# Optimization experiments

Hardware: AMD Instinct MI355X
Metric: run time of the kernel (lower is better)

Reference implementation:

```python
import jax, jax.numpy as jnp
import numpy as np

B, S, E, H = 64, 256, 1024, 16
D = E // H  # head dim = 64


def setup_inputs() -> dict:
    key = jax.random.key(0)
    ks = jax.random.split(key, 6)
    x = jax.random.normal(ks[0], (B, S, E), dtype=jnp.float32)
    # torch nn.MultiheadAttention packed in-projection [3E, E] and biases
    sc = 1.0 / np.sqrt(E)
    in_proj_w = jax.random.normal(ks[1], (3 * E, E), dtype=jnp.float32) * sc
    in_proj_b = jax.random.normal(ks[2], (3 * E,), dtype=jnp.float32) * 0.02
    out_proj_w = jax.random.normal(ks[3], (E, E), dtype=jnp.float32) * sc
    out_proj_b = jax.random.normal(ks[4], (E,), dtype=jnp.float32) * 0.02
    # spatial bias = exp(-dist^2 / (2*median)) in (0, 1], symmetric
    pos = jax.random.normal(ks[5], (S, 3), dtype=jnp.float32)
    dist = jnp.sqrt(jnp.sum((pos[:, None, :] - pos[None, :, :]) ** 2, -1) + 1e-12)
    med = jnp.median(dist)
    spatial_bias = jnp.exp(-dist ** 2 / (2.0 * med))
    return {"x": x, "in_proj_w": in_proj_w, "in_proj_b": in_proj_b,
            "out_proj_w": out_proj_w, "out_proj_b": out_proj_b,
            "spatial_bias": spatial_bias}


def reference(x, in_proj_w, in_proj_b, out_proj_w, out_proj_b, spatial_bias):
    # packed QKV projection: x [B,S,E] @ in_proj_w.T [E,3E]
    qkv = x @ in_proj_w.T + in_proj_b          # [B,S,3E]
    q, k, v = jnp.split(qkv, 3, axis=-1)       # each [B,S,E]
    q = q.reshape(B, S, H, D)
    k = k.reshape(B, S, H, D)
    v = v.reshape(B, S, H, D)
    scale = 1.0 / jnp.sqrt(jnp.asarray(D, dtype=x.dtype))
    # additive float attn_mask broadcast over batch & heads
    scores = jnp.einsum('bqhd,bkhd->bhqk', q, k) * scale + spatial_bias[None, None]
    attn = jax.nn.softmax(scores, axis=-1)     # [B,H,S,S]
    ctx = jnp.einsum('bhqk,bkhd->bqhd', attn, v).reshape(B, S, E)
    h = ctx @ out_proj_w.T + out_proj_b        # [B,S,E]
    return x + h
```

## Files before the change

kernel.cpp:

```cpp
#include <hip/hip_runtime.h>
#include <hip/hip_bf16.h>
#include <stdint.h>


typedef __attribute__((ext_vector_type(8))) __bf16 bf16x8;
typedef __attribute__((ext_vector_type(4))) float f32x4;

#define DEVI static __device__ __forceinline__

DEVI unsigned short f2bf(float f) {
  union { float f; unsigned u; } x; x.f = f;
  unsigned r = x.u + 0x7fffu + ((x.u >> 16) & 1u);
  return (unsigned short)(r >> 16);
}

typedef unsigned int __attribute__((address_space(1))) u32_g;
typedef unsigned int __attribute__((address_space(3))) u32_l;

DEVI void g2l16(const unsigned short* g, unsigned short* l) {
  __builtin_amdgcn_global_load_lds((const u32_g*)g, (u32_l*)l, 16, 0, 0);
}

__global__ __launch_bounds__(256) void cvt_kernel(const float* __restrict__ s,
                                                  unsigned short* __restrict__ d, int n) {
  int i = (blockIdx.x * 256 + threadIdx.x) * 4;
  if (i >= n) return;
  float4 v = *(const float4*)(s + i);
  ushort4 o;
  o.x = f2bf(v.x); o.y = f2bf(v.y); o.z = f2bf(v.z); o.w = f2bf(v.w);
  *(ushort4*)(d + i) = o;
}

template <int EPI>
__global__ __launch_bounds__(512, 2)
void gemm8(const unsigned short* __restrict__ A,
           const unsigned short* __restrict__ Bw,
           const float* __restrict__ bias,
           unsigned short* __restrict__ Qo,
           unsigned short* __restrict__ Ko,
           unsigned short* __restrict__ VTo,
           const float* __restrict__ Xres,
           float* __restrict__ Out) {
  extern __shared__ unsigned short lds[];
  const int lane = threadIdx.x & 63, wid = threadIdx.x >> 6;
  const int l15 = lane & 15, lg = lane >> 4;
  const int wr = wid >> 2, wcn = wid & 3;
  const int am0 = blockIdx.x * 256, bn0 = blockIdx.y * 256;

  const int srow0 = wid * 16 + (lane >> 2);
  const int scb0  = (lane & 3) * 16;

  f32x4 acc[8][4] = {};

#define SWZ(row) ((((row) >> 1) & 3) << 4)

#define STAGE(s) { \
    const int slot_ = (s) & 3; \
    _Pragma("unroll") \
    for (int j = 0; j < 2; ++j) { \
      const int row_ = j * 128 + srow0; \
      const int cs_ = scb0 ^ SWZ(row_); \
      g2l16(A  + (size_t)(am0 + row_) * 1024 + (s) * 32 + (cs_ >> 1), \
            &lds[slot_ * 8192 + j * 4096 + wid * 512]); \
      g2l16(Bw + (size_t)(bn0 + row_) * 1024 + (s) * 32 + (cs_ >> 1), \
            &lds[32768 + slot_ * 8192 + j * 4096 + wid * 512]); \
    } }

#define LOADFRAGS(p) \
    bf16x8 a[8], b[4]; \
    { const unsigned short* As_ = &lds[((p) & 3) * 8192]; \
      const unsigned short* Bs_ = &lds[32768 + ((p) & 3) * 8192]; \
      _Pragma("unroll") \
      for (int mf = 0; mf < 8; ++mf) { \
        const int row_ = wr * 128 + mf * 16 + l15; \
        a[mf] = *(const bf16x8*)((const char*)As_ + row_ * 64 + ((lg * 16) ^ SWZ(row_))); \
      } \
      _Pragma("unroll") \
      for (int nf = 0; nf < 4; ++nf) { \
        const int row_ = wcn * 64 + nf * 16 + l15; \
        b[nf] = *(const bf16x8*)((const char*)Bs_ + row_ * 64 + ((lg * 16) ^ SWZ(row_))); \
      } }

#define MFMAS() { \
    __builtin_amdgcn_s_setprio(1); \
    _Pragma("unroll") \
    for (int mf = 0; mf < 8; ++mf) \
      _Pragma("unroll") \
      for (int nf = 0; nf < 4; ++nf) \
        acc[mf][nf] = __builtin_amdgcn_mfma_f32_16x16x32_bf16(a[mf], b[nf], acc[mf][nf], 0, 0, 0); \
    __builtin_amdgcn_s_setprio(0); }

  STAGE(0) STAGE(1) STAGE(2)
  asm volatile("s_waitcnt vmcnt(8)" ::: "memory");
  __builtin_amdgcn_s_barrier();

#pragma unroll 4
  for (int p = 0; p < 29; ++p) {
    LOADFRAGS(p)
    STAGE(p + 3)
    asm volatile("s_waitcnt vmcnt(8)" ::: "memory");
    asm volatile("s_waitcnt lgkmcnt(0)" ::: "memory");
    __builtin_amdgcn_s_barrier();
    MFMAS()
  }
  { LOADFRAGS(29)
    asm volatile("s_waitcnt vmcnt(4)" ::: "memory");
    asm volatile("s_waitcnt lgkmcnt(0)" ::: "memory");
    __builtin_amdgcn_s_barrier();
    MFMAS() }
  { LOADFRAGS(30)
    asm volatile("s_waitcnt vmcnt(0)" ::: "memory");
    asm volatile("s_waitcnt lgkmcnt(0)" ::: "memory");
    __builtin_amdgcn_s_barrier();
    MFMAS() }
  { LOADFRAGS(31)
    MFMAS() }

  if (EPI == 0) {
#pragma unroll
    for (int nf = 0; nf < 4; ++nf) {
      const int col = bn0 + wcn * 64 + nf * 16 + l15;
      const int which = col >> 10;
      const int e = col & 1023;
      const int hh = e >> 6, dd = e & 63;
      const float bv = bias[col];
#pragma unroll
      for (int mf = 0; mf < 8; ++mf) {
        const int row0 = am0 + wr * 128 + mf * 16 + lg * 4;
        const int bb = row0 >> 8;
        const int s0 = row0 & 255;
        if (which == 2) {
          unsigned long long pk = 0;
#pragma unroll
          for (int r = 0; r < 4; ++r)
            pk |= (unsigned long long)f2bf(acc[mf][nf][r] + bv) << (16 * r);
          *(unsigned long long*)&VTo[((size_t)(bb * 16 + hh) * 64 + dd) * 256 + s0] = pk;
        } else {
          unsigned short* dst = (which == 0) ? Qo : Ko;
#pragma unroll
          for (int r = 0; r < 4; ++r)
            dst[((size_t)(bb * 16 + hh) * 256 + s0 + r) * 64 + dd] = f2bf(acc[mf][nf][r] + bv);
        }
      }
    }
  } else {
#pragma unroll
    for (int nf = 0; nf < 4; ++nf) {
      const int col = bn0 + wcn * 64 + nf * 16 + l15;
      const float bv = bias[col];
#pragma unroll
      for (int mf = 0; mf < 8; ++mf) {
#pragma unroll
        for (int r = 0; r < 4; ++r) {
          const int row = am0 + wr * 128 + mf * 16 + lg * 4 + r;
          const size_t idx = (size_t)row * 1024 + col;
          Out[idx] = Xres[idx] + acc[mf][nf][r] + bv;
        }
      }
    }
  }
#undef SWZ
#undef STAGE
#undef LOADFRAGS
#undef MFMAS
}

__global__ __launch_bounds__(256) void attn_kernel(const unsigned short* __restrict__ Qg,
                                                   const unsigned short* __restrict__ Kg,
                                                   const unsigned short* __restrict__ VTg,
                                                   const float* __restrict__ bias,
                                                   unsigned short* __restrict__ ctx) {
  __shared__ unsigned short P[4][64][80];
  const int lane = threadIdx.x & 63, wave = threadIdx.x >> 6;
  const int l15 = lane & 15, lg = lane >> 4;
  const int bh = blockIdx.x;
  const int bb = bh >> 4, hh = bh & 15;
  const size_t base = (size_t)bh * (256 * 64);
  const int q0 = wave * 64;

  bf16x8 qfr[4][2];
#pragma unroll
  for (int qi = 0; qi < 4; ++qi)
#pragma unroll
    for (int kc = 0; kc < 2; ++kc)
      qfr[qi][kc] = *(const bf16x8*)&Qg[base + (size_t)(q0 + qi * 16 + l15) * 64 + kc * 32 + lg * 8];

  f32x4 o[4][4] = {};
  float mrow[4], lrow[4];
#pragma unroll
  for (int i = 0; i < 4; ++i) { mrow[i] = -1e30f; lrow[i] = 0.f; }

  for (int c = 0; c < 4; ++c) {
    bf16x8 kfr[4][2];
#pragma unroll
    for (int kr = 0; kr < 4; ++kr)
#pragma unroll
      for (int kc = 0; kc < 2; ++kc)
        kfr[kr][kc] = *(const bf16x8*)&Kg[base + (size_t)(c * 64 + kr * 16 + l15) * 64 + kc * 32 + lg * 8];

    f32x4 s[4][4] = {};
#pragma unroll
    for (int kr = 0; kr < 4; ++kr)
#pragma unroll
      for (int qi = 0; qi < 4; ++qi)
#pragma unroll
        for (int kc = 0; kc < 2; ++kc)
          s[kr][qi] = __builtin_amdgcn_mfma_f32_16x16x32_bf16(kfr[kr][kc], qfr[qi][kc], s[kr][qi], 0, 0, 0);

    float cmax[4];
#pragma unroll
    for (int qi = 0; qi < 4; ++qi) cmax[qi] = -1e30f;
#pragma unroll
    for (int kr = 0; kr < 4; ++kr)
#pragma unroll
      for (int qi = 0; qi < 4; ++qi) {
        const int krow0 = c * 64 + kr * 16 + lg * 4;
        const int qcol = q0 + qi * 16 + l15;
        const f32x4 b4 = *(const f32x4*)&bias[qcol * 256 + krow0];
#pragma unroll
        for (int r = 0; r < 4; ++r) {
          float v = s[kr][qi][r] * 0.125f + b4[r];
          s[kr][qi][r] = v;
          cmax[qi] = fmaxf(cmax[qi], v);
        }
      }
#pragma unroll
    for (int qi = 0; qi < 4; ++qi) {
      cmax[qi] = fmaxf(cmax[qi], __shfl_xor(cmax[qi], 16, 64));
      cmax[qi] = fmaxf(cmax[qi], __shfl_xor(cmax[qi], 32, 64));
    }
    float resc[4], csum[4];
#pragma unroll
    for (int qi = 0; qi < 4; ++qi) {
      float mn = fmaxf(mrow[qi], cmax[qi]);
      resc[qi] = __expf(mrow[qi] - mn);
      mrow[qi] = mn;
      csum[qi] = 0.f;
    }
#pragma unroll
    for (int kr = 0; kr < 4; ++kr)
#pragma unroll
      for (int qi = 0; qi < 4; ++qi)
#pragma unroll
        for (int r = 0; r < 4; ++r) {
          float e = __expf(s[kr][qi][r] - mrow[qi]);
          s[kr][qi][r] = e;
          csum[qi] += e;
        }
#pragma unroll
    for (int qi = 0; qi < 4; ++qi) {
      csum[qi] += __shfl_xor(csum[qi], 16, 64);
      csum[qi] += __shfl_xor(csum[qi], 32, 64);
      lrow[qi] = lrow[qi] * resc[qi] + csum[qi];
    }

#pragma unroll
    for (int kr = 0; kr < 4; ++kr)
#pragma unroll
      for (int qi = 0; qi < 4; ++qi)
#pragma unroll
        for (int r = 0; r < 4; ++r)
          P[wave][qi * 16 + l15][kr * 16 + lg * 4 + r] = f2bf(s[kr][qi][r]);
    asm volatile("s_waitcnt lgkmcnt(0)" ::: "memory");

#pragma unroll
    for (int qrf = 0; qrf < 4; ++qrf)
#pragma unroll
      for (int r = 0; r < 4; ++r) {
        float f = __shfl(resc[qrf], lg * 4 + r, 64);
#pragma unroll
        for (int df = 0; df < 4; ++df) o[qrf][df][r] *= f;
      }

    bf16x8 vb[2][4], pa[4][2];
#pragma unroll
    for (int kc = 0; kc < 2; ++kc)
#pragma unroll
      for (int df = 0; df < 4; ++df)
        vb[kc][df] = *(const bf16x8*)&VTg[base + (size_t)(df * 16 + l15) * 256 + c * 64 + kc * 32 + lg * 8];
#pragma unroll
    for (int qrf = 0; qrf < 4; ++qrf)
#pragma unroll
      for (int kc = 0; kc < 2; ++kc)
        pa[qrf][kc] = *(const bf16x8*)&P[wave][qrf * 16 + l15][kc * 32 + lg * 8];
#pragma unroll
    for (int qrf = 0; qrf < 4; ++qrf)
#pragma unroll
      for (int df = 0; df < 4; ++df)
#pragma unroll
        for (int kc = 0; kc < 2; ++kc)
          o[qrf][df] = __builtin_amdgcn_mfma_f32_16x16x32_bf16(pa[qrf][kc], vb[kc][df], o[qrf][df], 0, 0, 0);
  }

#pragma unroll
  for (int qrf = 0; qrf < 4; ++qrf)
#pragma unroll
    for (int r = 0; r < 4; ++r) {
      float li = __shfl(lrow[qrf], lg * 4 + r, 64);
      float inv = 1.0f / li;
      const int q = q0 + qrf * 16 + lg * 4 + r;
#pragma unroll
      for (int df = 0; df < 4; ++df) {
        const int d = df * 16 + l15;
        ctx[((size_t)(bb * 256 + q) * 16 + hh) * 64 + d] = f2bf(o[qrf][df][r] * inv);
      }
    }
}

extern "C" void kernel_launch(void* const* d_in, const int* in_sizes, int n_in,
                              void* d_out, int out_size, void* d_ws, size_t ws_size,
                              hipStream_t stream) {
  const float* x  = (const float*)d_in[0];
  const float* wi = (const float*)d_in[1];
  const float* bi = (const float*)d_in[2];
  const float* wo = (const float*)d_in[3];
  const float* bo = (const float*)d_in[4];
  const float* sb = (const float*)d_in[5];
  float* out = (float*)d_out;

  char* ws = (char*)d_ws;
  unsigned short* xbf  = (unsigned short*)(ws);
  unsigned short* winb = (unsigned short*)(ws + 33554432u);
  unsigned short* wob  = (unsigned short*)(ws + 39845888u);
  unsigned short* Qb   = (unsigned short*)(ws + 41943040u);
  unsigned short* Kb   = (unsigned short*)(ws + 75497472u);
  unsigned short* VTb  = (unsigned short*)(ws + 109051904u);
  unsigned short* ctx  = xbf;

  (void)hipFuncSetAttribute(reinterpret_cast<const void*>(gemm8<0>),
                            hipFuncAttributeMaxDynamicSharedMemorySize, 131072);
  (void)hipFuncSetAttribute(reinterpret_cast<const void*>(gemm8<1>),
                            hipFuncAttributeMaxDynamicSharedMemorySize, 131072);

  cvt_kernel<<<16384, 256, 0, stream>>>(x, xbf, 16777216);
  cvt_kernel<<<3072, 256, 0, stream>>>(wi, winb, 3145728);
  cvt_kernel<<<1024, 256, 0, stream>>>(wo, wob, 1048576);

  gemm8<0><<<dim3(64, 12), 512, 131072, stream>>>(xbf, winb, bi, Qb, Kb, VTb, nullptr, nullptr);

  attn_kernel<<<1024, 256, 0, stream>>>(Qb, Kb, VTb, sb, ctx);

  gemm8<1><<<dim3(64, 4), 512, 131072, stream>>>(ctx, wob, bo, nullptr, nullptr, nullptr, x, out);
}
```

Before: 292.8 us.

## Double-buffer GEMM register fragments to overlap LDS reads with MFMAs

The GEMM main loop now keeps two sets of A/B register fragments and loads the next k-step's fragments from LDS while the MFMAs for the current step run. Before, every step waited on lgkmcnt(0) before starting its MFMAs. The aim is to hide LDS read latency behind matrix work. In exchange it roughly doubles fragment register use, which could cost occupancy or cause spills, and the barrier and slot-reuse ordering of the 4-slot ring has to stay correct.

Measured after the change: 406.4 us. 38.8% more time.

```diff
diff --git a/kernel.cpp b/kernel.cpp
--- a/kernel.cpp
+++ b/kernel.cpp
@@ -51,6 +51,7 @@
   const int scb0  = (lane & 3) * 16;
 
   f32x4 acc[8][4] = {};
+  bf16x8 aA[8], bA[4], aB[8], bB[4];
 
 #define SWZ(row) ((((row) >> 1) & 3) << 4)
 
@@ -66,55 +67,54 @@
             &lds[32768 + slot_ * 8192 + j * 4096 + wid * 512]); \
     } }
 
-#define LOADFRAGS(p) \
-    bf16x8 a[8], b[4]; \
-    { const unsigned short* As_ = &lds[((p) & 3) * 8192]; \
-      const unsigned short* Bs_ = &lds[32768 + ((p) & 3) * 8192]; \
-      _Pragma("unroll") \
-      for (int mf = 0; mf < 8; ++mf) { \
-        const int row_ = wr * 128 + mf * 16 + l15; \
-        a[mf] = *(const bf16x8*)((const char*)As_ + row_ * 64 + ((lg * 16) ^ SWZ(row_))); \
-      } \
-      _Pragma("unroll") \
-      for (int nf = 0; nf < 4; ++nf) { \
-        const int row_ = wcn * 64 + nf * 16 + l15; \
-        b[nf] = *(const bf16x8*)((const char*)Bs_ + row_ * 64 + ((lg * 16) ^ SWZ(row_))); \
-      } }
-
-#define MFMAS() { \
+#define LOADF(AF, BF, p) { \
+    const unsigned short* As_ = &lds[((p) & 3) * 8192]; \
+    const unsigned short* Bs_ = &lds[32768 + ((p) & 3) * 8192]; \
+    _Pragma("unroll") \
+    for (int mf = 0; mf < 8; ++mf) { \
+      const int row_ = wr * 128 + mf * 16 + l15; \
+      AF[mf] = *(const bf16x8*)((const char*)As_ + row_ * 64 + ((lg * 16) ^ SWZ(row_))); \
+    } \
+    _Pragma("unroll") \
+    for (int nf = 0; nf < 4; ++nf) { \
+      const int row_ = wcn * 64 + nf * 16 + l15; \
+      BF[nf] = *(const bf16x8*)((const char*)Bs_ + row_ * 64 + ((lg * 16) ^ SWZ(row_))); \
+    } }
+
+#define MFMAS(AF, BF) { \
     __builtin_amdgcn_s_setprio(1); \
     _Pragma("unroll") \
     for (int mf = 0; mf < 8; ++mf) \
       _Pragma("unroll") \
       for (int nf = 0; nf < 4; ++nf) \
-        acc[mf][nf] = __builtin_amdgcn_mfma_f32_16x16x32_bf16(a[mf], b[nf], acc[mf][nf], 0, 0, 0); \
+        acc[mf][nf] = __builtin_amdgcn_mfma_f32_16x16x32_bf16(AF[mf], BF[nf], acc[mf][nf], 0, 0, 0); \
     __builtin_amdgcn_s_setprio(0); }
+
+#define PHASE(p, AC, BC, AN, BN, DOSTAGE, VM) { \
+    if (DOSTAGE) STAGE((p) + 3) \
+    asm volatile("s_waitcnt vmcnt(" #VM ")" ::: "memory"); \
+    __builtin_amdgcn_s_barrier(); \
+    LOADF(AN, BN, (p) + 1) \
+    MFMAS(AC, BC) \
+    asm volatile("s_waitcnt lgkmcnt(0)" ::: "memory"); \
+    __builtin_amdgcn_sched_barrier(0); }
 
   STAGE(0) STAGE(1) STAGE(2)
   asm volatile("s_waitcnt vmcnt(8)" ::: "memory");
   __builtin_amdgcn_s_barrier();
-
-#pragma unroll 4
-  for (int p = 0; p < 29; ++p) {
-    LOADFRAGS(p)
-    STAGE(p + 3)
-    asm volatile("s_waitcnt vmcnt(8)" ::: "memory");
-    asm volatile("s_waitcnt lgkmcnt(0)" ::: "memory");
-    __builtin_amdgcn_s_barrier();
-    MFMAS()
+  LOADF(aA, bA, 0)
+  asm volatile("s_waitcnt lgkmcnt(0)" ::: "memory");
+  __builtin_amdgcn_sched_barrier(0);
+
+#pragma unroll 2
+  for (int p = 0; p < 28; p += 2) {
+    PHASE(p,     aA, bA, aB, bB, 1, 8)
+    PHASE(p + 1, aB, bB, aA, bA, 1, 8)
   }
-  { LOADFRAGS(29)
-    asm volatile("s_waitcnt vmcnt(4)" ::: "memory");
-    asm volatile("s_waitcnt lgkmcnt(0)" ::: "memory");
-    __builtin_amdgcn_s_barrier();
-    MFMAS() }
-  { LOADFRAGS(30)
-    asm volatile("s_waitcnt vmcnt(0)" ::: "memory");
-    asm volatile("s_waitcnt lgkmcnt(0)" ::: "memory");
-    __builtin_amdgcn_s_barrier();
-    MFMAS() }
-  { LOADFRAGS(31)
-    MFMAS() }
+  PHASE(28, aA, bA, aB, bB, 1, 8)
+  PHASE(29, aB, bB, aA, bA, 0, 4)
+  PHASE(30, aA, bA, aB, bB, 0, 0)
+  MFMAS(aB, bB)
 
   if (EPI == 0) {
 #pragma unroll
@@ -161,8 +161,9 @@
   }
 #undef SWZ
 #undef STAGE
-#undef LOADFRAGS
+#undef LOADF
 #undef MFMAS
+#undef PHASE
 }
 
 __global__ __launch_bounds__(256) void attn_kernel(const unsigned short* __restrict__ Qg,
```
